# Kernel optimization log

Hardware: AMD Instinct MI355X
Metric: run time of the kernel (lower is better)

## Reference

```python
import jax, jax.numpy as jnp
import numpy as np

BETA = 0.25


def setup_inputs() -> dict:
    key = jax.random.key(0)
    k1, k2 = jax.random.split(key)
    z = jax.random.normal(k1, (8, 256, 8, 16, 16), dtype=jnp.float32)
    # nn.Embedding initialized uniform(-1/n_e, 1/n_e)
    n_e, e_dim = 8192, 256
    emb = jax.random.uniform(k2, (n_e, e_dim), dtype=jnp.float32,
                             minval=-1.0 / n_e, maxval=1.0 / n_e)
    return {"z": z, "emb": emb}


def reference(z, emb):
    # z: [b, c, d, h, w]; emb: [n_e, c]
    b, c, d, h, w = z.shape
    zp = jnp.transpose(z, (0, 2, 3, 4, 1))          # b d h w c
    zf = zp.reshape(-1, c)                           # [N, c]
    # squared euclidean distances: ||z||^2 + ||e||^2 - 2 z.e
    dist = (jnp.sum(zf * zf, axis=1, keepdims=True)
            + jnp.sum(emb * emb, axis=1)
            - 2.0 * jnp.einsum('nc,kc->nk', zf, emb))  # [N, n_e]
    idx = jnp.argmin(dist, axis=1)                   # [N]
    z_q = emb[idx].reshape(zp.shape)                 # b d h w c
    # legacy=True loss
    loss = (jnp.mean((jax.lax.stop_gradient(z_q) - zp) ** 2)
            + BETA * jnp.mean((z_q - jax.lax.stop_gradient(zp)) ** 2))
    # straight-through estimator
    z_q = zp + jax.lax.stop_gradient(z_q - zp)
    z_q = jnp.transpose(z_q, (0, 4, 1, 2, 3))        # b c d h w
    return z_q, loss, idx
```

## Files before the change

### kernel.cpp

```cpp
#include <hip/hip_runtime.h>

#define NROWS 16384
#define NE 8192
#define NCH 64
#define CHK 128
#define OUT_LOSS 4194304
#define OUT_IDX  4194305

#define U_MARGIN  2.5e-5f
#define CH_MARGIN 3.0e-5f

typedef __attribute__((ext_vector_type(8))) short short8;
typedef __attribute__((ext_vector_type(8))) unsigned short u16x8;
typedef __attribute__((ext_vector_type(4))) float f32x4;

__device__ inline unsigned short bf16_rne(float f) {
    unsigned u = __float_as_uint(f);
    return (unsigned short)((u + 0x7FFFu + ((u >> 16) & 1u)) >> 16);
}

__device__ inline float np_dist(const float4* __restrict__ zf4,
                                const float4* __restrict__ ef, float s1v) {
#pragma clang fp contract(off)
    float a0 = 0.f, a1 = 0.f, a2 = 0.f, a3 = 0.f;
#pragma unroll
    for (int u = 0; u < 64; ++u) {
        float4 e4 = ef[u];
        float4 zz = zf4[u];
        float p0 = zz.x * e4.x; asm("" : "+v"(p0)); a0 += p0;
        float p1 = zz.y * e4.y; asm("" : "+v"(p1)); a1 += p1;
        float p2 = zz.z * e4.z; asm("" : "+v"(p2)); a2 += p2;
        float p3 = zz.w * e4.w; asm("" : "+v"(p3)); a3 += p3;
    }
    float t1 = a0 + a1;
    float t2 = a2 + a3;
    float Pn = t1 + t2;
    return s1v - 2.0f * Pn;
}

__global__ void k_s1(const float* __restrict__ Z, float* __restrict__ S1) {
#pragma clang fp contract(off)
    const int n = blockIdx.x * 256 + threadIdx.x;
    const int b = n >> 11, m = n & 2047;
    const float* zp = Z + b * 524288 + m;
    float blk[2];
#pragma unroll
    for (int h = 0; h < 2; ++h) {
        float r[8];
#pragma unroll
        for (int j = 0; j < 8; ++j) {
            float z = zp[(h * 128 + j) * 2048];
            float w = z * z;
            asm("" : "+v"(w));
            r[j] = w;
        }
        for (int t2 = 1; t2 < 16; ++t2) {
#pragma unroll
            for (int j = 0; j < 8; ++j) {
                float z = zp[(h * 128 + t2 * 8 + j) * 2048];
                float w = z * z;
                asm("" : "+v"(w));
                r[j] += w;
            }
        }
        float s01 = r[0] + r[1], s23 = r[2] + r[3];
        float s45 = r[4] + r[5], s67 = r[6] + r[7];
        blk[h] = (s01 + s23) + (s45 + s67);
    }
    S1[n] = blk[0] + blk[1];
}

__global__ void k_prep_z(const float* __restrict__ Z, float* __restrict__ Zt,
                         unsigned short* __restrict__ Zh, unsigned short* __restrict__ Zl) {
    __shared__ float tile[32][33];
    const int blk = blockIdx.x;
    const int mt = blk & 63;
    const int ct = (blk >> 6) & 7;
    const int b  = blk >> 9;
    const int t = threadIdx.x, tr = t >> 5, tc = t & 31;
#pragma unroll
    for (int rr = 0; rr < 4; ++rr) {
        int cl = tr + rr * 8;
        tile[cl][tc] = Z[b * 524288 + (ct * 32 + cl) * 2048 + mt * 32 + tc];
    }
    __syncthreads();
#pragma unroll
    for (int rr = 0; rr < 4; ++rr) {
        int nl = tr + rr * 8;
        float x = tile[tc][nl];
        unsigned short h = bf16_rne(x);
        float hf = __uint_as_float((unsigned)h << 16);
        unsigned short lo = bf16_rne(x - hf);
        int n = b * 2048 + mt * 32 + nl;
        Zt[n * 256 + ct * 32 + tc] = x;
        Zh[n * 256 + ct * 32 + tc] = h;
        Zl[n * 256 + ct * 32 + tc] = lo;
    }
}

__global__ void k_prep_e(const float* __restrict__ E, unsigned short* __restrict__ Eh,
                         unsigned short* __restrict__ El) {
    const int g = blockIdx.x * 256 + threadIdx.x;
    float4 v = reinterpret_cast<const float4*>(E)[g];
    ushort4 h, lo;
    h.x = bf16_rne(v.x); h.y = bf16_rne(v.y); h.z = bf16_rne(v.z); h.w = bf16_rne(v.w);
    lo.x = bf16_rne(v.x - __uint_as_float((unsigned)h.x << 16));
    lo.y = bf16_rne(v.y - __uint_as_float((unsigned)h.y << 16));
    lo.z = bf16_rne(v.z - __uint_as_float((unsigned)h.z << 16));
    lo.w = bf16_rne(v.w - __uint_as_float((unsigned)h.w << 16));
    reinterpret_cast<ushort4*>(Eh)[g] = h;
    reinterpret_cast<ushort4*>(El)[g] = lo;
}

#define SM_A_H 0
#define SM_A_L 16384
#define SM_B_H 32768
#define SM_B_L 49152
__launch_bounds__(256, 2)
__global__ void k_screen(const unsigned short* __restrict__ Zh, const unsigned short* __restrict__ Zl,
                         const unsigned short* __restrict__ Eh, const unsigned short* __restrict__ El,
                         float4* __restrict__ partrec) {
    __shared__ __align__(16) char lds[65536];
    __shared__ float sm1[2][128];
    __shared__ float sm2[2][128];
    __shared__ int   sk1[2][128];
    const int t = threadIdx.x;
    const int nt = blockIdx.x >> 6;
    const int kt = blockIdx.x & 63;
    const int n0 = nt * 128, k0 = kt * 128;
    const int w = t >> 6, l = t & 63;
    const int wm = w >> 1, wn = w & 1;

    f32x4 acc[4][4];
#pragma unroll
    for (int i = 0; i < 4; ++i)
#pragma unroll
        for (int j = 0; j < 4; ++j) acc[i][j] = (f32x4)(0.0f);

    const int r = t >> 1;
    const int gbase = (t & 1) * 4;

    for (int kb = 0; kb < 4; ++kb) {
        const int c0 = kb * 64;
        if (kb) __syncthreads();
#pragma unroll
        for (int i = 0; i < 4; ++i) {
            const int g16 = gbase + i;
            const int off = r * 128 + ((g16 << 4) ^ ((r & 7) << 4));
            const int ge = c0 + g16 * 8;
            *(u16x8*)(lds + SM_A_H + off) = *(const u16x8*)(Zh + (n0 + r) * 256 + ge);
            *(u16x8*)(lds + SM_A_L + off) = *(const u16x8*)(Zl + (n0 + r) * 256 + ge);
            *(u16x8*)(lds + SM_B_H + off) = *(const u16x8*)(Eh + (k0 + r) * 256 + ge);
            *(u16x8*)(lds + SM_B_L + off) = *(const u16x8*)(El + (k0 + r) * 256 + ge);
        }
        __syncthreads();
#pragma unroll
        for (int ks = 0; ks < 2; ++ks) {
            const int cb = ks * 64 + ((l >> 4) << 4);
            short8 ah[4], al[4], bh[4], bl[4];
#pragma unroll
            for (int mf = 0; mf < 4; ++mf) {
                const int ar = wm * 64 + mf * 16 + (l & 15);
                const int off = ar * 128 + (cb ^ ((ar & 7) << 4));
                ah[mf] = *(const short8*)(lds + SM_A_H + off);
                al[mf] = *(const short8*)(lds + SM_A_L + off);
            }
#pragma unroll
            for (int nf = 0; nf < 4; ++nf) {
                const int br = wn * 64 + nf * 16 + (l & 15);
                const int off = br * 128 + (cb ^ ((br & 7) << 4));
                bh[nf] = *(const short8*)(lds + SM_B_H + off);
                bl[nf] = *(const short8*)(lds + SM_B_L + off);
            }
#pragma unroll
            for (int mf = 0; mf < 4; ++mf)
#pragma unroll
                for (int nf = 0; nf < 4; ++nf) {
                    acc[mf][nf] = __builtin_amdgcn_mfma_f32_16x16x32_bf16(ah[mf], bh[nf], acc[mf][nf], 0, 0, 0);
                    acc[mf][nf] = __builtin_amdgcn_mfma_f32_16x16x32_bf16(ah[mf], bl[nf], acc[mf][nf], 0, 0, 0);
                    acc[mf][nf] = __builtin_amdgcn_mfma_f32_16x16x32_bf16(al[mf], bh[nf], acc[mf][nf], 0, 0, 0);
                }
        }
    }

#pragma unroll
    for (int mf = 0; mf < 4; ++mf) {
#pragma unroll
        for (int q = 0; q < 4; ++q) {
            float m1 = -acc[mf][0][q];
            int kk1 = wn * 64 + (l & 15);
            float m2 = INFINITY;
#pragma unroll
            for (int nf = 1; nf < 4; ++nf) {
                float v = -acc[mf][nf][q];
                int c = wn * 64 + nf * 16 + (l & 15);
                if (v < m1) { m2 = m1; m1 = v; kk1 = c; }
                else m2 = fminf(m2, v);
            }
#pragma unroll
            for (int o = 1; o < 16; o <<= 1) {
                float om1 = __shfl_xor(m1, o);
                float om2 = __shfl_xor(m2, o);
                int   ok  = __shfl_xor(kk1, o);
                float hi = fmaxf(m1, om1);
                if (om1 < m1) { kk1 = ok; m1 = om1; }
                m2 = fminf(fminf(m2, om2), hi);
            }
            if ((l & 15) == 0) {
                const int rowl = wm * 64 + mf * 16 + ((l >> 4) << 2) + q;
                sm1[wn][rowl] = m1; sm2[wn][rowl] = m2; sk1[wn][rowl] = kk1;
            }
        }
    }
    __syncthreads();
    if (t < 128) {
        float a1 = sm1[0][t], a2 = sm2[0][t]; int ak = sk1[0][t];
        float b1 = sm1[1][t], b2 = sm2[1][t]; int bk = sk1[1][t];
        float hi = fmaxf(a1, b1);
        float m1 = a1; int kk = ak;
        if (b1 < a1) { m1 = b1; kk = bk; }
        float m2 = fminf(fminf(a2, b2), hi);
        partrec[(size_t)(n0 + t) * NCH + kt] =
            make_float4(m1, m2, __int_as_float(k0 + kk), 0.0f);
    }
}

__global__ void k_rescue(const float* __restrict__ Zt, const float* __restrict__ E,
                         const float* __restrict__ S1, const float4* __restrict__ partrec,
                         int* __restrict__ idxv, double* __restrict__ dmin,
                         float* __restrict__ out) {
#pragma clang fp contract(off)
    __shared__ __align__(16) float zsm[4][256];
    const int t = threadIdx.x;
    const int r = t >> 6;
    const int lane = t & 63;
    const int n = blockIdx.x * 4 + r;

    reinterpret_cast<float4*>(zsm[r])[lane] =
        reinterpret_cast<const float4*>(Zt)[(size_t)n * 64 + lane];
    __syncthreads();

    const float4* zf4 = reinterpret_cast<const float4*>(zsm[r]);
    const float s1v = S1[n];

    float4 rec = partrec[(size_t)n * NCH + lane];
    float pm1 = rec.x, pm2 = rec.y;
    int pk = __float_as_int(rec.z);

    float rowm = pm1;
#pragma unroll
    for (int o = 1; o < 64; o <<= 1) rowm = fminf(rowm, __shfl_xor(rowm, o));

    unsigned long long best = 0xFFFFFFFFFFFFFFFFull;

    if (pm1 <= rowm + U_MARGIN) {
        const float4* ef = reinterpret_cast<const float4*>(E + (size_t)pk * 256);
        float d = np_dist(zf4, ef, s1v);
        best = ((unsigned long long)__float_as_uint(d) << 32) | (unsigned)pk;
    }

    unsigned long long qm = __ballot(pm2 <= rowm + CH_MARGIN);
    while (qm) {
        const int ch = __ffsll(qm) - 1;
        qm &= qm - 1;
        const int c0 = ch * CHK;
#pragma unroll 1
        for (int s = 0; s < 2; ++s) {
            const int k = c0 + s * 64 + lane;
            const float4* ef = reinterpret_cast<const float4*>(E + (size_t)k * 256);
            float ax = 0.f, ay = 0.f, az = 0.f, aw = 0.f;
#pragma unroll
            for (int u = 0; u < 64; ++u) {
                float4 e4 = ef[u];
                float4 zz = zf4[u];
                ax = fmaf(zz.x, e4.x, ax);
                ay = fmaf(zz.y, e4.y, ay);
                az = fmaf(zz.z, e4.z, az);
                aw = fmaf(zz.w, e4.w, aw);
            }
            const float uk = -((ax + ay) + (az + aw));
            if (uk <= rowm + U_MARGIN) {
                float d = np_dist(zf4, ef, s1v);
                unsigned long long pkd =
                    ((unsigned long long)__float_as_uint(d) << 32) | (unsigned)k;
                if (pkd < best) best = pkd;
            }
        }
    }

#pragma unroll
    for (int o = 32; o; o >>= 1) {
        unsigned lo = (unsigned)(best & 0xFFFFFFFFull);
        unsigned hi = (unsigned)(best >> 32);
        unsigned olo = __shfl_xor(lo, o);
        unsigned ohi = __shfl_xor(hi, o);
        unsigned long long ob = ((unsigned long long)ohi << 32) | olo;
        if (ob < best) best = ob;
    }
    const int besti = (int)(best & 0xFFFFFFFFull);

    {
        float4 e4 = reinterpret_cast<const float4*>(E + (size_t)besti * 256)[lane];
        float4 zz = zf4[lane];
        double d0 = (double)zz.x - (double)e4.x;
        double d1 = (double)zz.y - (double)e4.y;
        double d2 = (double)zz.z - (double)e4.z;
        double d3 = (double)zz.w - (double)e4.w;
        double d = d0 * d0 + d1 * d1 + d2 * d2 + d3 * d3;
#pragma unroll
        for (int o = 32; o; o >>= 1) d += __shfl_xor(d, o);
        if (lane == 0) {
            idxv[n] = besti;
            out[OUT_IDX + n] = (float)besti;
            dmin[n] = d;
        }
    }
}

__global__ void k_gather(const float* __restrict__ emb, const int* __restrict__ idxv,
                         float* __restrict__ out) {
    __shared__ float tile[32][33];
    __shared__ int kidx[32];
    const int blk = blockIdx.x;
    const int ct = blk & 7;
    const int mt = (blk >> 3) & 63;
    const int b = blk >> 9;
    const int t = threadIdx.x, tr = t >> 5, tc = t & 31;

    if (t < 32) kidx[t] = idxv[b * 2048 + mt * 32 + t];
    __syncthreads();
#pragma unroll
    for (int rr = 0; rr < 4; ++rr) {
        int row = tr + rr * 8;
        tile[row][tc] = emb[kidx[row] * 256 + ct * 32 + tc];
    }
    __syncthreads();
#pragma unroll
    for (int rr = 0; rr < 4; ++rr) {
        int cl = tr + rr * 8;
        out[b * 524288 + (ct * 32 + cl) * 2048 + mt * 32 + tc] = tile[tc][cl];
    }
}

__global__ void k_loss(const double* __restrict__ dmin, float* __restrict__ out) {
    __shared__ double sm[256];
    double s = 0.0;
    for (int i = threadIdx.x; i < NROWS; i += 256) s += dmin[i];
    sm[threadIdx.x] = s;
    __syncthreads();
    for (int o = 128; o; o >>= 1) {
        if (threadIdx.x < o) sm[threadIdx.x] += sm[threadIdx.x + o];
        __syncthreads();
    }
    if (threadIdx.x == 0)
        out[OUT_LOSS] = (float)(1.25 * sm[0] / 4194304.0);
}

extern "C" void kernel_launch(void* const* d_in, const int* in_sizes, int n_in,
                              void* d_out, int out_size, void* d_ws, size_t ws_size,
                              hipStream_t stream) {
    const float* Z = (const float*)d_in[0];
    const float* E = (const float*)d_in[1];
    float* out = (float*)d_out;
    char* ws = (char*)d_ws;

    size_t o = 0;
    float*  S1      = (float*)(ws + o);  o += 64 << 10;
    double* dmin    = (double*)(ws + o); o += 128 << 10;
    int*    idxv    = (int*)(ws + o);    o += 64 << 10;
    float4* partrec = (float4*)(ws + o); o += (size_t)NROWS * NCH * 16;
    float*  Zt      = (float*)(ws + o);  o += (size_t)NROWS * 256 * 4;
    unsigned short* Zh = (unsigned short*)(ws + o); o += (size_t)NROWS * 256 * 2;
    unsigned short* Zl = (unsigned short*)(ws + o); o += (size_t)NROWS * 256 * 2;
    unsigned short* Eh = (unsigned short*)(ws + o); o += (size_t)NE * 256 * 2;
    unsigned short* El = (unsigned short*)(ws + o); o += (size_t)NE * 256 * 2;

    hipLaunchKernelGGL(k_prep_z, dim3(4096), dim3(256), 0, stream, Z, Zt, Zh, Zl);
    hipLaunchKernelGGL(k_prep_e, dim3(2048), dim3(256), 0, stream, E, Eh, El);
    hipLaunchKernelGGL(k_s1,     dim3(64),   dim3(256), 0, stream, Z, S1);
    hipLaunchKernelGGL(k_screen, dim3(8192), dim3(256), 0, stream, Zh, Zl, Eh, El, partrec);
    hipLaunchKernelGGL(k_rescue, dim3(4096), dim3(256), 0, stream, Zt, E, S1,
                       partrec, idxv, dmin, out);
    hipLaunchKernelGGL(k_gather, dim3(4096), dim3(256), 0, stream, E, idxv, out);
    hipLaunchKernelGGL(k_loss,   dim3(1),    dim3(256), 0, stream, dmin, out);
}
```

Before: 572.2 us.

## Keep Z tile in registers across codebook sweep and fold S1 into rescue

The screening kernel now loads each 128-row Z tile's hi/lo bf16 fragments into registers once and loops over 1024 codebook entries per block, streaming only E tiles through LDS. This removes the repeated loading of Z per codebook tile and cuts the grid from 8192 to 1024 blocks. The separate k_s1 kernel, which read Z with strided accesses, is removed, and the row norm is recomputed inside k_rescue from the Z row already staged in shared memory, using the same summation order. The trade-off is much higher register pressure from holding A fragments, and fewer blocks available to hide latency.

```diff
diff --git a/kernel.cpp b/kernel.cpp
--- a/kernel.cpp
+++ b/kernel.cpp
@@ -36,38 +36,6 @@
     float t2 = a2 + a3;
     float Pn = t1 + t2;
     return s1v - 2.0f * Pn;
-}
-
-__global__ void k_s1(const float* __restrict__ Z, float* __restrict__ S1) {
-#pragma clang fp contract(off)
-    const int n = blockIdx.x * 256 + threadIdx.x;
-    const int b = n >> 11, m = n & 2047;
-    const float* zp = Z + b * 524288 + m;
-    float blk[2];
-#pragma unroll
-    for (int h = 0; h < 2; ++h) {
-        float r[8];
-#pragma unroll
-        for (int j = 0; j < 8; ++j) {
-            float z = zp[(h * 128 + j) * 2048];
-            float w = z * z;
-            asm("" : "+v"(w));
-            r[j] = w;
-        }
-        for (int t2 = 1; t2 < 16; ++t2) {
-#pragma unroll
-            for (int j = 0; j < 8; ++j) {
-                float z = zp[(h * 128 + t2 * 8 + j) * 2048];
-                float w = z * z;
-                asm("" : "+v"(w));
-                r[j] += w;
-            }
-        }
-        float s01 = r[0] + r[1], s23 = r[2] + r[3];
-        float s45 = r[4] + r[5], s67 = r[6] + r[7];
-        blk[h] = (s01 + s23) + (s45 + s67);
-    }
-    S1[n] = blk[0] + blk[1];
 }
 
 __global__ void k_prep_z(const float* __restrict__ Z, float* __restrict__ Zt,
@@ -112,121 +80,114 @@
     reinterpret_cast<ushort4*>(El)[g] = lo;
 }
 
-#define SM_A_H 0
-#define SM_A_L 16384
-#define SM_B_H 32768
-#define SM_B_L 49152
 __launch_bounds__(256, 2)
 __global__ void k_screen(const unsigned short* __restrict__ Zh, const unsigned short* __restrict__ Zl,
                          const unsigned short* __restrict__ Eh, const unsigned short* __restrict__ El,
                          float4* __restrict__ partrec) {
-    __shared__ __align__(16) char lds[65536];
-    __shared__ float sm1[2][128];
-    __shared__ float sm2[2][128];
-    __shared__ int   sk1[2][128];
+    __shared__ __align__(16) char lds[32768];
     const int t = threadIdx.x;
-    const int nt = blockIdx.x >> 6;
-    const int kt = blockIdx.x & 63;
-    const int n0 = nt * 128, k0 = kt * 128;
+    const int kr = blockIdx.x & 7;
+    const int nt = blockIdx.x >> 3;
+    const int n0 = nt * 128;
     const int w = t >> 6, l = t & 63;
-    const int wm = w >> 1, wn = w & 1;
-
-    f32x4 acc[4][4];
-#pragma unroll
-    for (int i = 0; i < 4; ++i)
-#pragma unroll
-        for (int j = 0; j < 4; ++j) acc[i][j] = (f32x4)(0.0f);
-
-    const int r = t >> 1;
-    const int gbase = (t & 1) * 4;
-
-    for (int kb = 0; kb < 4; ++kb) {
-        const int c0 = kb * 64;
-        if (kb) __syncthreads();
-#pragma unroll
-        for (int i = 0; i < 4; ++i) {
-            const int g16 = gbase + i;
-            const int off = r * 128 + ((g16 << 4) ^ ((r & 7) << 4));
-            const int ge = c0 + g16 * 8;
-            *(u16x8*)(lds + SM_A_H + off) = *(const u16x8*)(Zh + (n0 + r) * 256 + ge);
-            *(u16x8*)(lds + SM_A_L + off) = *(const u16x8*)(Zl + (n0 + r) * 256 + ge);
-            *(u16x8*)(lds + SM_B_H + off) = *(const u16x8*)(Eh + (k0 + r) * 256 + ge);
-            *(u16x8*)(lds + SM_B_L + off) = *(const u16x8*)(El + (k0 + r) * 256 + ge);
-        }
+    const int l15 = l & 15, lh = l >> 4;
+
+    short8 Ah[2][8], Al[2][8];
+#pragma unroll
+    for (int mf = 0; mf < 2; ++mf) {
+        const size_t rowoff = (size_t)(n0 + w * 32 + mf * 16 + l15) * 256 + lh * 8;
+#pragma unroll
+        for (int s = 0; s < 8; ++s) {
+            Ah[mf][s] = *(const short8*)(Zh + rowoff + s * 32);
+            Al[mf][s] = *(const short8*)(Zl + rowoff + s * 32);
+        }
+    }
+
+    f32x4 acc[2][8];
+#pragma unroll
+    for (int mf = 0; mf < 2; ++mf)
+#pragma unroll
+        for (int nf = 0; nf < 8; ++nf) acc[mf][nf] = (f32x4)(0.0f);
+
+    for (int step = 0; step < 32; ++step) {
+        const int kt = step >> 2, kb = step & 3;
+        const int k0 = kr * 1024 + kt * 128;
+
         __syncthreads();
+        u16x8 breg[8];
+#pragma unroll
+        for (int i = 0; i < 8; ++i) {
+            const int gid = i * 256 + t;
+            const int row = (gid >> 3) & 127, gc = gid & 7;
+            const unsigned short* src = (gid >> 10 ? El : Eh);
+            breg[i] = *(const u16x8*)(src + (size_t)(k0 + row) * 256 + kb * 64 + gc * 8);
+        }
+#pragma unroll
+        for (int i = 0; i < 8; ++i) {
+            const int gid = i * 256 + t;
+            const int arr = gid >> 10, row = (gid >> 3) & 127, gc = gid & 7;
+            *(u16x8*)(lds + arr * 16384 + row * 128 + ((gc * 16) ^ ((row & 7) << 4))) = breg[i];
+        }
+        __syncthreads();
+
 #pragma unroll
         for (int ks = 0; ks < 2; ++ks) {
-            const int cb = ks * 64 + ((l >> 4) << 4);
-            short8 ah[4], al[4], bh[4], bl[4];
-#pragma unroll
-            for (int mf = 0; mf < 4; ++mf) {
-                const int ar = wm * 64 + mf * 16 + (l & 15);
-                const int off = ar * 128 + (cb ^ ((ar & 7) << 4));
-                ah[mf] = *(const short8*)(lds + SM_A_H + off);
-                al[mf] = *(const short8*)(lds + SM_A_L + off);
+            const int cb = ks * 64 + (lh << 4);
+            const int s = kb * 2 + ks;
+#pragma unroll
+            for (int nf = 0; nf < 8; ++nf) {
+                const int br = nf * 16 + l15;
+                const int off = br * 128 + (cb ^ ((br & 7) << 4));
+                short8 bh = *(const short8*)(lds + off);
+                short8 bl = *(const short8*)(lds + 16384 + off);
+#pragma unroll
+                for (int mf = 0; mf < 2; ++mf) {
+                    acc[mf][nf] = __builtin_amdgcn_mfma_f32_16x16x32_bf16(Ah[mf][s], bh, acc[mf][nf], 0, 0, 0);
+                    acc[mf][nf] = __builtin_amdgcn_mfma_f32_16x16x32_bf16(Ah[mf][s], bl, acc[mf][nf], 0, 0, 0);
+                    acc[mf][nf] = __builtin_amdgcn_mfma_f32_16x16x32_bf16(Al[mf][s], bh, acc[mf][nf], 0, 0, 0);
+                }
             }
-#pragma unroll
-            for (int nf = 0; nf < 4; ++nf) {
-                const int br = wn * 64 + nf * 16 + (l & 15);
-                const int off = br * 128 + (cb ^ ((br & 7) << 4));
-                bh[nf] = *(const short8*)(lds + SM_B_H + off);
-                bl[nf] = *(const short8*)(lds + SM_B_L + off);
+        }
+
+        if (kb == 3) {
+            const int kbase = k0 + l15;
+#pragma unroll
+            for (int mf = 0; mf < 2; ++mf) {
+#pragma unroll
+                for (int q = 0; q < 4; ++q) {
+                    float m1 = -acc[mf][0][q];
+                    int k1 = kbase;
+                    float m2 = INFINITY;
+#pragma unroll
+                    for (int nf = 1; nf < 8; ++nf) {
+                        float v = -acc[mf][nf][q];
+                        if (v < m1) { m2 = m1; m1 = v; k1 = kbase + nf * 16; }
+                        else m2 = fminf(m2, v);
+                    }
+#pragma unroll
+                    for (int o = 1; o < 16; o <<= 1) {
+                        float om1 = __shfl_xor(m1, o);
+                        float om2 = __shfl_xor(m2, o);
+                        int   ok  = __shfl_xor(k1, o);
+                        float hi = fmaxf(m1, om1);
+                        if (om1 < m1) { m1 = om1; k1 = ok; }
+                        m2 = fminf(fminf(m2, om2), hi);
+                    }
+                    if (l15 == 0) {
+                        const int n = n0 + w * 32 + mf * 16 + lh * 4 + q;
+                        partrec[(size_t)n * NCH + (kr * 8 + kt)] =
+                            make_float4(m1, m2, __int_as_float(k1), 0.0f);
+                    }
+                }
+#pragma unroll
+                for (int nf = 0; nf < 8; ++nf) acc[mf][nf] = (f32x4)(0.0f);
             }
-#pragma unroll
-            for (int mf = 0; mf < 4; ++mf)
-#pragma unroll
-                for (int nf = 0; nf < 4; ++nf) {
-                    acc[mf][nf] = __builtin_amdgcn_mfma_f32_16x16x32_bf16(ah[mf], bh[nf], acc[mf][nf], 0, 0, 0);
-                    acc[mf][nf] = __builtin_amdgcn_mfma_f32_16x16x32_bf16(ah[mf], bl[nf], acc[mf][nf], 0, 0, 0);
-                    acc[mf][nf] = __builtin_amdgcn_mfma_f32_16x16x32_bf16(al[mf], bh[nf], acc[mf][nf], 0, 0, 0);
-                }
-        }
-    }
-
-#pragma unroll
-    for (int mf = 0; mf < 4; ++mf) {
-#pragma unroll
-        for (int q = 0; q < 4; ++q) {
-            float m1 = -acc[mf][0][q];
-            int kk1 = wn * 64 + (l & 15);
-            float m2 = INFINITY;
-#pragma unroll
-            for (int nf = 1; nf < 4; ++nf) {
-                float v = -acc[mf][nf][q];
-                int c = wn * 64 + nf * 16 + (l & 15);
-                if (v < m1) { m2 = m1; m1 = v; kk1 = c; }
-                else m2 = fminf(m2, v);
-            }
-#pragma unroll
-            for (int o = 1; o < 16; o <<= 1) {
-                float om1 = __shfl_xor(m1, o);
-                float om2 = __shfl_xor(m2, o);
-                int   ok  = __shfl_xor(kk1, o);
-                float hi = fmaxf(m1, om1);
-                if (om1 < m1) { kk1 = ok; m1 = om1; }
-                m2 = fminf(fminf(m2, om2), hi);
-            }
-            if ((l & 15) == 0) {
-                const int rowl = wm * 64 + mf * 16 + ((l >> 4) << 2) + q;
-                sm1[wn][rowl] = m1; sm2[wn][rowl] = m2; sk1[wn][rowl] = kk1;
-            }
-        }
-    }
-    __syncthreads();
-    if (t < 128) {
-        float a1 = sm1[0][t], a2 = sm2[0][t]; int ak = sk1[0][t];
-        float b1 = sm1[1][t], b2 = sm2[1][t]; int bk = sk1[1][t];
-        float hi = fmaxf(a1, b1);
-        float m1 = a1; int kk = ak;
-        if (b1 < a1) { m1 = b1; kk = bk; }
-        float m2 = fminf(fminf(a2, b2), hi);
-        partrec[(size_t)(n0 + t) * NCH + kt] =
-            make_float4(m1, m2, __int_as_float(k0 + kk), 0.0f);
+        }
     }
 }
 
 __global__ void k_rescue(const float* __restrict__ Zt, const float* __restrict__ E,
-                         const float* __restrict__ S1, const float4* __restrict__ partrec,
+                         const float4* __restrict__ partrec,
                          int* __restrict__ idxv, double* __restrict__ dmin,
                          float* __restrict__ out) {
 #pragma clang fp contract(off)
@@ -241,7 +202,22 @@
     __syncthreads();
 
     const float4* zf4 = reinterpret_cast<const float4*>(zsm[r]);
-    const float s1v = S1[n];
+
+    float ch = 0.0f;
+    if (lane < 16) {
+        const int h = lane >> 3, j = lane & 7;
+        for (int t2 = 0; t2 < 16; ++t2) {
+            float z = zsm[r][h * 128 + t2 * 8 + j];
+            float w = z * z;
+            asm("" : "+v"(w));
+            ch += w;
+        }
+    }
+    ch += __shfl_xor(ch, 1);
+    ch += __shfl_xor(ch, 2);
+    ch += __shfl_xor(ch, 4);
+    ch += __shfl_xor(ch, 8);
+    const float s1v = __shfl(ch, 0);
 
     float4 rec = partrec[(size_t)n * NCH + lane];
     float pm1 = rec.x, pm2 = rec.y;
@@ -261,9 +237,9 @@
 
     unsigned long long qm = __ballot(pm2 <= rowm + CH_MARGIN);
     while (qm) {
-        const int ch = __ffsll(qm) - 1;
+        const int chk = __ffsll(qm) - 1;
         qm &= qm - 1;
-        const int c0 = ch * CHK;
+        const int c0 = chk * CHK;
 #pragma unroll 1
         for (int s = 0; s < 2; ++s) {
             const int k = c0 + s * 64 + lane;
@@ -365,7 +341,6 @@
     char* ws = (char*)d_ws;
 
     size_t o = 0;
-    float*  S1      = (float*)(ws + o);  o += 64 << 10;
     double* dmin    = (double*)(ws + o); o += 128 << 10;
     int*    idxv    = (int*)(ws + o);    o += 64 << 10;
     float4* partrec = (float4*)(ws + o); o += (size_t)NROWS * NCH * 16;
@@ -377,9 +352,8 @@
 
     hipLaunchKernelGGL(k_prep_z, dim3(4096), dim3(256), 0, stream, Z, Zt, Zh, Zl);
     hipLaunchKernelGGL(k_prep_e, dim3(2048), dim3(256), 0, stream, E, Eh, El);
-    hipLaunchKernelGGL(k_s1,     dim3(64),   dim3(256), 0, stream, Z, S1);
-    hipLaunchKernelGGL(k_screen, dim3(8192), dim3(256), 0, stream, Zh, Zl, Eh, El, partrec);
-    hipLaunchKernelGGL(k_rescue, dim3(4096), dim3(256), 0, stream, Zt, E, S1,
+    hipLaunchKernelGGL(k_screen, dim3(1024), dim3(256), 0, stream, Zh, Zl, Eh, El, partrec);
+    hipLaunchKernelGGL(k_rescue, dim3(4096), dim3(256), 0, stream, Zt, E,
                        partrec, idxv, dmin, out);
     hipLaunchKernelGGL(k_gather, dim3(4096), dim3(256), 0, stream, E, idxv, out);
     hipLaunchKernelGGL(k_loss,   dim3(1),    dim3(256), 0, stream, dmin, out);
```

Result: slower. 586.5 us (+2.5%).
